# Kernel tuning notes

Measured on AMD Instinct MI355X. Metric: run time of the kernel, lower is better.

The kernel has to match this reference:

```python
import jax, jax.numpy as jnp
import numpy as np

B, F, D, C, K = 131072, 32, 16, 64, 8  # batch, features, qsvt degree, classes, KAN grid
CLIP = 1.0 - 1e-6


def setup_inputs() -> dict:
    key = jax.random.key(0)
    ks = jax.random.split(key, 7)
    return {
        "X": jax.random.normal(ks[0], (B, F), jnp.float32),
        "qsvt_phases": 0.1 * jax.random.normal(ks[1], (D,), jnp.float32),
        "lcu_weights": jax.random.uniform(ks[2], (F, D), jnp.float32),
        "sum_scale": jnp.ones((F,), jnp.float32) + 0.1 * jax.random.normal(ks[3], (F,), jnp.float32),
        "sum_bias": 0.1 * jax.random.normal(ks[4], (F,), jnp.float32),
        "kan_coeff": jax.random.normal(ks[5], (C, F, K), jnp.float32) / np.sqrt(F * K),
        "kan_bias": jnp.zeros((C,), jnp.float32),
    }


def reference(X, qsvt_phases, lcu_weights, sum_scale, sum_bias, kan_coeff, kan_bias):
    # QSVT: Chebyshev-with-phases polynomial features of each scalar input,
    # vectorized over (batch, feature) instead of the original Python loops.
    degree = qsvt_phases.shape[0]
    grid = kan_coeff.shape[-1]
    theta = jnp.arccos(jnp.clip(X, -CLIP, CLIP))                  # [B,F]
    kd = jnp.arange(1, degree + 1, dtype=X.dtype)                 # [D]
    qsvt_vecs = jnp.cos(theta[..., None] * kd + qsvt_phases)      # [B,F,D]
    # LCU block: normalized linear combination over the degree axis -> scalar per (b,f)
    lcu = jnp.sum(qsvt_vecs * lcu_weights, axis=-1) / (
        jnp.sum(jnp.abs(lcu_weights), axis=-1) + 1e-6)            # [B,F]
    # QuantumSumBlock (one per feature): per-feature affine + tanh squash
    feat = jnp.tanh(sum_scale * lcu + sum_bias)                   # [B,F]
    # KAN layer: Chebyshev basis expansion then per-(class,feature,basis) coefficients
    t2 = jnp.arccos(jnp.clip(feat, -CLIP, CLIP))                  # [B,F]
    kk = jnp.arange(grid, dtype=X.dtype)                          # [K]
    basis = jnp.cos(t2[..., None] * kk)                           # [B,F,K]
    return jnp.einsum('bfk,cfk->bc', basis, kan_coeff) + kan_bias  # [B,C]
```

## Files before the change

### kernel.cpp

```cpp
#include <hip/hip_runtime.h>

#define F 32
#define Dd 16
#define C 64
#define Kk 8
#define CLIPV (1.0f - 1e-6f)
#define K2 2.8853900817779268f
#define NBLK 1024
#define MT 2

typedef short v8s __attribute__((ext_vector_type(8)));
typedef float v4f __attribute__((ext_vector_type(4)));
typedef float v2f __attribute__((ext_vector_type(2)));

static __device__ inline unsigned cvtpk(float lo, float hi) {
    unsigned r;
    asm("v_cvt_pk_bf16_f32 %0, %1, %2" : "=v"(r) : "v"(lo), "v"(hi));
    return r;
}

static __device__ inline v2f pk_sub(v2f a, v2f b) {
    v2f r;
    asm("v_pk_add_f32 %0, %1, %2 neg_lo:[0,1] neg_hi:[0,1]"
        : "=v"(r) : "v"(a), "v"(b));
    return r;
}
static __device__ inline v2f pk_fma(v2f a, v2f b, v2f c) {
    v2f r;
    asm("v_pk_fma_f32 %0, %1, %2, %3"
        : "=v"(r) : "v"(a), "v"(b), "v"(c));
    return r;
}

#define BAR_WRITES() do {                                        \
    asm volatile("s_waitcnt lgkmcnt(0)" ::: "memory");           \
    __builtin_amdgcn_s_barrier();                                \
    asm volatile("" ::: "memory");                               \
} while (0)
#define BAR_READS() do {                                         \
    asm volatile("" ::: "memory");                               \
    __builtin_amdgcn_s_barrier();                                \
    asm volatile("" ::: "memory");                               \
} while (0)

__global__ __launch_bounds__(256, 4) void qkan_kernel(
    const float* __restrict__ X,
    const float* __restrict__ phases,
    const float* __restrict__ lcu_w,
    const float* __restrict__ sscale,
    const float* __restrict__ sbias,
    const float* __restrict__ coeff,
    const float* __restrict__ kbias,
    float* __restrict__ out)
{
    __shared__ unsigned short s_basis[F * 512];

    const int tid = threadIdx.x;
    const int lane = tid & 63;
    const int wu = __builtin_amdgcn_readfirstlane(tid >> 6);
    const int h = lane >> 4;
    const int r16 = lane & 15;
    const int fe = tid & 31;
    const int fe7 = fe & 7;
    const int rg = tid >> 5;

    const int rb0 = blockIdx.x * (MT * 64);

    float xq[8];
    {
        const float* xp = X + (size_t)(rb0 + rg * 8) * F + fe;
#pragma unroll
        for (int m = 0; m < 8; ++m) xq[m] = xp[m * F];
    }

    v2f cc[16];
    float fbias;
    {
        const float* lwf = lcu_w + fe * Dd;
        float wv[16];
        float asum = 0.f;
#pragma unroll
        for (int d = 0; d < Dd; ++d) {
            wv[d] = lwf[d];
            asum += fabsf(wv[d]);
        }
        const float sc = K2 * sscale[fe] / (asum + 1e-6f);
#pragma unroll
        for (int d = 0; d < Dd; ++d) {
            float sp, cp;
            __sincosf(phases[d], &sp, &cp);
            cc[d][0] = sc * wv[d] * cp;
            cc[d][1] = -sc * wv[d] * sp;
        }
        fbias = K2 * sbias[fe];
    }

    v8s Bfr[8];
    const int cidx = wu * 16 + r16;
#pragma unroll
    for (int q = 0; q < 8; ++q) {
        const float* gp = coeff + ((size_t)(cidx * F + 4 * q + h) * Kk);
        const float4 g0 = *reinterpret_cast<const float4*>(gp);
        const float4 g1 = *reinterpret_cast<const float4*>(gp + 4);
        union { unsigned u[4]; v8s v; } bb;
        bb.u[0] = cvtpk(g0.x, g0.y);
        bb.u[1] = cvtpk(g0.z, g0.w);
        bb.u[2] = cvtpk(g1.x, g1.y);
        bb.u[3] = cvtpk(g1.z, g1.w);
        Bfr[q] = bb.v;
    }
    const float biasreg = kbias[cidx];

    for (int mt = 0; mt < MT; ++mt) {
        const int row_base = rb0 + mt * 64;
        if (mt) BAR_READS();

        float xn[8];
        if (mt + 1 < MT) {
            const float* xp = X + (size_t)(row_base + 64 + rg * 8) * F + fe;
#pragma unroll
            for (int m = 0; m < 8; ++m) xn[m] = xp[m * F];
        }

#pragma unroll
        for (int m = 0; m < 8; ++m) {
            const float x = __builtin_amdgcn_fmed3f(xq[m], -CLIPV, CLIPV);
            const float s1 = __builtin_amdgcn_sqrtf(__builtin_fmaf(-x, x, 1.f));
            const float tx = x + x;
            const v2f tx2 = {tx, tx};
            v2f w = {0.f, 0.f}, wp = {0.f, 0.f};
#pragma unroll
            for (int j = 15; j >= 0; --j) {
                const v2f wn = pk_fma(tx2, w, pk_sub(cc[j], wp));
                wp = w;
                w = wn;
            }
            float z = fbias - wp[0];
            z = __builtin_fmaf(x, w[0], z);
            z = __builtin_fmaf(s1, w[1], z);
            float e;
            asm("v_exp_f32 %0, %1" : "=v"(e) : "v"(z));
            const float rr = __builtin_amdgcn_rcpf(e + 1.f);
            const float t = __builtin_fmaf(-2.f, rr, 1.f);
            const float t2 = t + t;
            const float b1 = t;
            const float b2 = t2 * b1 - 1.f;
            const float b3 = t2 * b2 - b1;
            const float b4 = t2 * b3 - b2;
            const float b5 = t2 * b4 - b3;
            const float b6 = t2 * b5 - b4;
            const float b7 = t2 * b6 - b5;
            uint4 pk;
            pk.x = cvtpk(1.f, b1);
            pk.y = cvtpk(b2, b3);
            pk.z = cvtpk(b4, b5);
            pk.w = cvtpk(b6, b7);
            *reinterpret_cast<uint4*>(
                &s_basis[fe * 512 + rg * 64 + ((m ^ fe7) << 3)]) = pk;
        }
        BAR_WRITES();

#pragma unroll
        for (int t = 0; t < 4; ++t) {
            const int s0 = ((t * 16 + r16) ^ h) << 3;
            v4f acc = {biasreg, biasreg, biasreg, biasreg};
#pragma unroll
            for (int q = 0; q < 8; ++q) {
                const int idx = (4 * q + h) * 512 + (s0 ^ ((q & 1) << 5));
                const v8s a = *reinterpret_cast<const v8s*>(&s_basis[idx]);
                acc = __builtin_amdgcn_mfma_f32_16x16x32_bf16(a, Bfr[q], acc, 0, 0, 0);
            }
            const int row0 = row_base + t * 16 + h * 4;
#pragma unroll
            for (int i = 0; i < 4; ++i) {
                out[(size_t)(row0 + i) * C + cidx] = acc[i];
            }
        }

        if (mt + 1 < MT) {
#pragma unroll
            for (int m = 0; m < 8; ++m) xq[m] = xn[m];
        }
    }
}

extern "C" void kernel_launch(void* const* d_in, const int* in_sizes, int n_in,
                              void* d_out, int out_size, void* d_ws, size_t ws_size,
                              hipStream_t stream) {
    const float* X  = (const float*)d_in[0];
    const float* ph = (const float*)d_in[1];
    const float* lw = (const float*)d_in[2];
    const float* ss = (const float*)d_in[3];
    const float* sb = (const float*)d_in[4];
    const float* kc = (const float*)d_in[5];
    const float* kb = (const float*)d_in[6];
    float* out = (float*)d_out;
    qkan_kernel<<<dim3(NBLK), dim3(256), 0, stream>>>(X, ph, lw, ss, sb, kc, kb, out);
}
```

Measured before the change: 26.17 us.

## Compute each wave's own tile before barrier and prefetch both X tiles

Each wave now runs the MFMA tile whose basis rows it wrote itself right after its own LDS writes complete. Only a local lgkmcnt wait is needed for that, and the block barrier is deferred to before the remaining three tiles, which lets waves overlap. Both X tiles are loaded at kernel start and the mt loop is unrolled, removing the mid-loop load and register copy. The phase sin/cos setup uses the raw hardware v_sin/v_cos instructions on pre-scaled arguments. This raises register pressure and issues global loads earlier.

Result: slower. 30.81 us (+17.7%).

```diff
diff --git a/kernel.cpp b/kernel.cpp
--- a/kernel.cpp
+++ b/kernel.cpp
@@ -6,6 +6,7 @@
 #define Kk 8
 #define CLIPV (1.0f - 1e-6f)
 #define K2 2.8853900817779268f
+#define INV2PI 0.15915494309189535f
 #define NBLK 1024
 #define MT 2
 
@@ -32,6 +33,10 @@
     return r;
 }
 
+#define WAIT_LGKM() do {                                         \
+    asm volatile("s_waitcnt lgkmcnt(0)" ::: "memory");           \
+    __builtin_amdgcn_sched_barrier(0);                           \
+} while (0)
 #define BAR_WRITES() do {                                        \
     asm volatile("s_waitcnt lgkmcnt(0)" ::: "memory");           \
     __builtin_amdgcn_s_barrier();                                \
@@ -66,11 +71,14 @@
 
     const int rb0 = blockIdx.x * (MT * 64);
 
-    float xq[8];
+    float xq[8], xn[8];
     {
-        const float* xp = X + (size_t)(rb0 + rg * 8) * F + fe;
-#pragma unroll
-        for (int m = 0; m < 8; ++m) xq[m] = xp[m * F];
+        const float* xp0 = X + (size_t)(rb0 + rg * 8) * F + fe;
+        const float* xp1 = xp0 + (size_t)64 * F;
+#pragma unroll
+        for (int m = 0; m < 8; ++m) xq[m] = xp0[m * F];
+#pragma unroll
+        for (int m = 0; m < 8; ++m) xn[m] = xp1[m * F];
     }
 
     v2f cc[16];
@@ -87,8 +95,10 @@
         const float sc = K2 * sscale[fe] / (asum + 1e-6f);
 #pragma unroll
         for (int d = 0; d < Dd; ++d) {
+            const float pr = phases[d] * INV2PI;
             float sp, cp;
-            __sincosf(phases[d], &sp, &cp);
+            asm("v_sin_f32 %0, %1" : "=v"(sp) : "v"(pr));
+            asm("v_cos_f32 %0, %1" : "=v"(cp) : "v"(pr));
             cc[d][0] = sc * wv[d] * cp;
             cc[d][1] = -sc * wv[d] * sp;
         }
@@ -111,20 +121,14 @@
     }
     const float biasreg = kbias[cidx];
 
+#pragma unroll
     for (int mt = 0; mt < MT; ++mt) {
         const int row_base = rb0 + mt * 64;
         if (mt) BAR_READS();
 
-        float xn[8];
-        if (mt + 1 < MT) {
-            const float* xp = X + (size_t)(row_base + 64 + rg * 8) * F + fe;
-#pragma unroll
-            for (int m = 0; m < 8; ++m) xn[m] = xp[m * F];
-        }
-
 #pragma unroll
         for (int m = 0; m < 8; ++m) {
-            const float x = __builtin_amdgcn_fmed3f(xq[m], -CLIPV, CLIPV);
+            const float x = __builtin_amdgcn_fmed3f(mt ? xn[m] : xq[m], -CLIPV, CLIPV);
             const float s1 = __builtin_amdgcn_sqrtf(__builtin_fmaf(-x, x, 1.f));
             const float tx = x + x;
             const v2f tx2 = {tx, tx};
@@ -158,11 +162,10 @@
             *reinterpret_cast<uint4*>(
                 &s_basis[fe * 512 + rg * 64 + ((m ^ fe7) << 3)]) = pk;
         }
-        BAR_WRITES();
-
-#pragma unroll
-        for (int t = 0; t < 4; ++t) {
-            const int s0 = ((t * 16 + r16) ^ h) << 3;
+
+        WAIT_LGKM();
+        {
+            const int s0 = ((wu * 16 + r16) ^ h) << 3;
             v4f acc = {biasreg, biasreg, biasreg, biasreg};
 #pragma unroll
             for (int q = 0; q < 8; ++q) {
@@ -170,16 +173,30 @@
                 const v8s a = *reinterpret_cast<const v8s*>(&s_basis[idx]);
                 acc = __builtin_amdgcn_mfma_f32_16x16x32_bf16(a, Bfr[q], acc, 0, 0, 0);
             }
-            const int row0 = row_base + t * 16 + h * 4;
+            const int row0 = row_base + wu * 16 + h * 4;
 #pragma unroll
             for (int i = 0; i < 4; ++i) {
                 out[(size_t)(row0 + i) * C + cidx] = acc[i];
             }
         }
-
-        if (mt + 1 < MT) {
-#pragma unroll
-            for (int m = 0; m < 8; ++m) xq[m] = xn[m];
+        BAR_WRITES();
+
+#pragma unroll
+        for (int k = 1; k < 4; ++k) {
+            const int t = (wu + k) & 3;
+            const int s0 = ((t * 16 + r16) ^ h) << 3;
+            v4f acc = {biasreg, biasreg, biasreg, biasreg};
+#pragma unroll
+            for (int q = 0; q < 8; ++q) {
+                const int idx = (4 * q + h) * 512 + (s0 ^ ((q & 1) << 5));
+                const v8s a = *reinterpret_cast<const v8s*>(&s_basis[idx]);
+                acc = __builtin_amdgcn_mfma_f32_16x16x32_bf16(a, Bfr[q], acc, 0, 0, 0);
+            }
+            const int row0 = row_base + t * 16 + h * 4;
+#pragma unroll
+            for (int i = 0; i < 4; ++i) {
+                out[(size_t)(row0 + i) * C + cidx] = acc[i];
+            }
         }
     }
 }
```
